# Performance work log

Measured on AMD Instinct MI355X. Metric: run time of the kernel, lower is better.

The kernel has to match this reference:

```python
import jax, jax.numpy as jnp
import numpy as np

C = 512   # in_channels
N = 256   # spatial side (H == W required by the bmm structure)


def setup_inputs() -> dict:
    key = jax.random.key(0)
    kx, kf, kg, kh = jax.random.split(key, 4)
    scale = 1.0 / np.sqrt(C)  # spectral-normalized 1x1 conv weights have ~unit spectral norm
    x = jax.random.normal(kx, (C, N, N), dtype=jnp.float32)
    Wf = jax.random.normal(kf, (C, C), dtype=jnp.float32) * scale  # 1x1 conv kernel squeezed
    Wg = jax.random.normal(kg, (C, C), dtype=jnp.float32) * scale
    Wh = jax.random.normal(kh, (C, C), dtype=jnp.float32) * scale
    return {"x": x, "Wf": Wf, "Wg": Wg, "Wh": Wh}


def reference(x, Wf, Wg, Wh):
    # 1x1 convs (no bias) == channel-mixing matmuls: out[c,h,w] = sum_k W[c,k] x[k,h,w]
    f = jnp.einsum('ck,khw->chw', Wf, x)
    g = jnp.einsum('ck,khw->chw', Wg, x)
    h = jnp.einsum('ck,khw->chw', Wh, x)
    # torch.bmm(f, g): per-channel HxW @ HxW matmul -> [C, N, N]
    scores = jnp.einsum('cik,ckj->cij', f, g)
    # nn.Softmax(dim=1) on [C, N, N] -> softmax over the row axis (axis=1)
    attn_map = jax.nn.softmax(scores, axis=1)
    # torch.bmm(h, attn_map) -> [C, N, N]
    attn = jnp.einsum('cik,ckj->cij', h, attn_map)
    return x + attn
```

## Files before the change

kernel.cpp:

```cpp
#include <hip/hip_runtime.h>

typedef unsigned short u16;
typedef unsigned int   u32;
typedef __attribute__((ext_vector_type(8))) _Float16 half8;
typedef __attribute__((ext_vector_type(4))) float f32x4;
typedef __attribute__((ext_vector_type(2))) float f32x2;
typedef __attribute__((ext_vector_type(4))) u32   u32x4;
typedef __attribute__((ext_vector_type(4))) unsigned short u16x4;

#define MFMAH __builtin_amdgcn_mfma_f32_16x16x32_f16

__device__ u16 W16[786432];

__device__ __forceinline__ u16 f2h(float f) {
  _Float16 h = (_Float16)f;
  union { _Float16 hh; u16 u; } cv; cv.hh = h; return cv.u;
}
__device__ __forceinline__ u32 pkh(float a, float b) {
  return (u32)f2h(a) | ((u32)f2h(b) << 16);
}
__device__ __forceinline__ void gload16(const void* g, void* l) {
  __builtin_amdgcn_global_load_lds(
      (const __attribute__((address_space(1))) void*)g,
      (__attribute__((address_space(3))) void*)l, 16, 0, 0);
}

__global__ __launch_bounds__(256)
void prep_w(const float* __restrict__ Wf, const float* __restrict__ Wg,
            const float* __restrict__ Wh)
{
  const int r = blockIdx.x;
  const int k = threadIdx.x * 2;
  const float* src = (r < 512) ? (Wf + (size_t)r * 512)
                   : (r < 1024) ? (Wg + (size_t)(r - 512) * 512)
                                : (Wh + (size_t)(r - 1024) * 512);
  f32x2 v = *(const f32x2*)(src + k);
  *(u32*)(W16 + (size_t)r * 512 + k) = pkh(v[0], v[1]);
}

__global__ __launch_bounds__(256)
void prep_x(const float* __restrict__ x, u16* __restrict__ x16)
{
  __shared__ float tile[64 * 256];
  const int bk = blockIdx.x & 7, bn = blockIdx.x >> 3;
  const int t = threadIdx.x;
  const int cw = (t & 63) * 4, r0 = (t >> 6) * 16;
#pragma unroll
  for (int it = 0; it < 16; ++it) {
    const int r = r0 + it;
    *(f32x4*)&tile[r * 256 + cw] =
        *(const f32x4*)(x + (size_t)(bk * 64 + r) * 65536 + (size_t)bn * 256 + cw);
  }
  __syncthreads();
  u32 w[32];
#pragma unroll
  for (int q = 0; q < 32; ++q)
    w[q] = pkh(tile[(2 * q) * 256 + t], tile[(2 * q + 1) * 256 + t]);
  const size_t ob = (size_t)(bn * 256 + t) * 512 + bk * 64;
#pragma unroll
  for (int c4 = 0; c4 < 8; ++c4)
    *(u32x4*)(x16 + ob + c4 * 8) = (u32x4){w[4*c4], w[4*c4+1], w[4*c4+2], w[4*c4+3]};
}

__global__ __launch_bounds__(256)
void conv_fgh(const u16* __restrict__ x16, u16* __restrict__ fb,
              u16* __restrict__ gTb, u16* __restrict__ hb)
{
  __shared__ u16 sA[4096], sB[4096];
  const int bid = blockIdx.x;
  const int xcd = bid & 7, idx = bid >> 3;
  const int tn = xcd * 64 + idx / 12;
  const int tm = idx % 12;
  const bool gmode = (tm >= 4) && (tm < 8);
  const int t = threadIdx.x, lane = t & 63, wid = t >> 6;
  const int wr = wid >> 1, wc = wid & 1, lr = lane & 15, lq = lane >> 4;

  const int row0 = t >> 2, row1 = 64 + (t >> 2);
  const int ks0 = (((t & 3) ^ ((row0 >> 1) & 3)) << 3);
  const int ks1 = (((t & 3) ^ ((row1 >> 1) & 3)) << 3);
  const int arA0 = tm * 128 + row0, arA1 = tm * 128 + row1;
  const int bxr0 = gmode ? ((((tn & 1) << 7) + row0) * 256 + (tn >> 1)) : (tn * 128 + row0);
  const int bxr1 = gmode ? ((((tn & 1) << 7) + row1) * 256 + (tn >> 1)) : (tn * 128 + row1);

  int offA[4], offB[4];
#pragma unroll
  for (int mi = 0; mi < 4; ++mi) {
    const int rowA = wr * 64 + mi * 16 + lr;
    offA[mi] = rowA * 32 + ((lq ^ ((rowA >> 1) & 3)) << 3);
  }
#pragma unroll
  for (int ni = 0; ni < 4; ++ni) {
    const int rowB = wc * 64 + ni * 16 + lr;
    offB[ni] = rowB * 32 + ((lq ^ ((rowB >> 1) & 3)) << 3);
  }

  f32x4 acc[4][4] = {};

  for (int k0 = 0; k0 < 512; k0 += 32) {
    gload16(W16 + (size_t)arA0 * 512 + k0 + ks0, (char*)sA + t * 16);
    gload16(W16 + (size_t)arA1 * 512 + k0 + ks1, (char*)sA + 4096 + t * 16);
    gload16(x16 + (size_t)bxr0 * 512 + k0 + ks0, (char*)sB + t * 16);
    gload16(x16 + (size_t)bxr1 * 512 + k0 + ks1, (char*)sB + 4096 + t * 16);
    __syncthreads();
    half8 a[4], b[4];
#pragma unroll
    for (int mi = 0; mi < 4; ++mi) a[mi] = *(const half8*)(sA + offA[mi]);
#pragma unroll
    for (int ni = 0; ni < 4; ++ni) b[ni] = *(const half8*)(sB + offB[ni]);
#pragma unroll
    for (int mi = 0; mi < 4; ++mi)
#pragma unroll
      for (int ni = 0; ni < 4; ++ni)
        acc[mi][ni] = MFMAH(a[mi], b[ni], acc[mi][ni], 0, 0, 0);
    __syncthreads();
  }

  u16* dst = gmode ? gTb : ((tm < 4) ? fb : hb);
  const int mloc = (tm < 4) ? tm : (gmode ? (tm - 4) : (tm - 8));
  const int rbase = mloc * 128 + wr * 64;
  const int cbase = tn * 128 + wc * 64;
#pragma unroll
  for (int mi = 0; mi < 4; ++mi)
#pragma unroll
    for (int ni = 0; ni < 4; ++ni) {
      const int r0 = rbase + mi * 16 + lq * 4;
      const int cc = cbase + ni * 16 + lr;
#pragma unroll
      for (int r = 0; r < 4; ++r)
        dst[(size_t)(r0 + r) * 65536 + cc] = f2h(acc[mi][ni][r]);
    }
}

__global__ __launch_bounds__(512)
void scores_kernel(const u16* __restrict__ fb, const u16* __restrict__ gTb,
                   u16* __restrict__ Pt)
{
  __shared__ u16 sA[8192];
  __shared__ u16 sB[4096];
  __shared__ float cmax[512], csum[512];
  const int bid = blockIdx.x;
  const int xcd = bid & 7, i2 = bid >> 3;
  const int c = xcd * 64 + (i2 >> 1), jt = i2 & 1;
  const size_t cb = (size_t)c * 65536;
  const int t = threadIdx.x, lane = t & 63, wid = t >> 6;
  const int wr = wid >> 1, wc = wid & 1, lr = lane & 15, lq = lane >> 4;

  const int arow0 = t >> 2, arow1 = 128 + (t >> 2);
  const int aks0 = (((t & 3) ^ ((arow0 >> 1) & 3)) << 3);
  const int aks1 = (((t & 3) ^ ((arow1 >> 1) & 3)) << 3);
  const int brow = t >> 2;
  const int bks  = (((t & 3) ^ ((brow >> 1) & 3)) << 3);

  int offA[4], offB[4];
#pragma unroll
  for (int mi = 0; mi < 4; ++mi) {
    const int rowA = wr * 64 + mi * 16 + lr;
    offA[mi] = rowA * 32 + ((lq ^ ((rowA >> 1) & 3)) << 3);
  }
#pragma unroll
  for (int ni = 0; ni < 4; ++ni) {
    const int rowB = wc * 64 + ni * 16 + lr;
    offB[ni] = rowB * 32 + ((lq ^ ((rowB >> 1) & 3)) << 3);
  }

  f32x4 acc[4][4] = {};

  for (int k0 = 0; k0 < 256; k0 += 32) {
    gload16(fb + cb + (size_t)arow0 * 256 + k0 + aks0, (char*)sA + t * 16);
    gload16(fb + cb + (size_t)arow1 * 256 + k0 + aks1, (char*)sA + 8192 + t * 16);
    gload16(gTb + cb + (size_t)(jt * 128 + brow) * 256 + k0 + bks, (char*)sB + t * 16);
    __syncthreads();
    half8 a[4], b[4];
#pragma unroll
    for (int mi = 0; mi < 4; ++mi) a[mi] = *(const half8*)(sA + offA[mi]);
#pragma unroll
    for (int ni = 0; ni < 4; ++ni) b[ni] = *(const half8*)(sB + offB[ni]);
#pragma unroll
    for (int mi = 0; mi < 4; ++mi)
#pragma unroll
      for (int ni = 0; ni < 4; ++ni)
        acc[mi][ni] = MFMAH(a[mi], b[ni], acc[mi][ni], 0, 0, 0);
    __syncthreads();
  }

#pragma unroll
  for (int ni = 0; ni < 4; ++ni) {
    const int col = wc * 64 + ni * 16 + lr;
    float m = -3.4e38f;
#pragma unroll
    for (int mi = 0; mi < 4; ++mi) {
      f32x4 a = acc[mi][ni];
      m = fmaxf(m, fmaxf(fmaxf(a[0], a[1]), fmaxf(a[2], a[3])));
    }
    m = fmaxf(m, __shfl_xor(m, 16));
    m = fmaxf(m, __shfl_xor(m, 32));
    cmax[wr * 128 + col] = m;
  }
  __syncthreads();
#pragma unroll
  for (int ni = 0; ni < 4; ++ni) {
    const int col = wc * 64 + ni * 16 + lr;
    const float M = fmaxf(fmaxf(cmax[col], cmax[128 + col]),
                          fmaxf(cmax[256 + col], cmax[384 + col]));
    float s = 0.f;
#pragma unroll
    for (int mi = 0; mi < 4; ++mi)
#pragma unroll
      for (int r = 0; r < 4; ++r) {
        float e = __expf(acc[mi][ni][r] - M);
        acc[mi][ni][r] = e; s += e;
      }
    s += __shfl_xor(s, 16);
    s += __shfl_xor(s, 32);
    csum[wr * 128 + col] = s;
  }
  __syncthreads();
#pragma unroll
  for (int ni = 0; ni < 4; ++ni) {
    const int col = wc * 64 + ni * 16 + lr;
    const float rs = 1.f / (csum[col] + csum[128 + col] + csum[256 + col] + csum[384 + col]);
    const int j = jt * 128 + col;
#pragma unroll
    for (int mi = 0; mi < 4; ++mi) {
      u16x4 w = { f2h(acc[mi][ni][0] * rs), f2h(acc[mi][ni][1] * rs),
                  f2h(acc[mi][ni][2] * rs), f2h(acc[mi][ni][3] * rs) };
      *(u16x4*)(Pt + cb + (size_t)j * 256 + wr * 64 + mi * 16 + lq * 4) = w;
    }
  }
}

__global__ __launch_bounds__(256)
void attn_kernel(const u16* __restrict__ hb, const u16* __restrict__ Pt,
                 const float* __restrict__ x, float* __restrict__ out)
{
  __shared__ u16 sA[128 * 32], sB[128 * 32];
  const int bid = blockIdx.x;
  const int wg = (bid & 7) * 256 + (bid >> 3);
  const int c = wg >> 2, tm = (wg >> 1) & 1, tn = wg & 1;
  const int t = threadIdx.x, lane = t & 63, wid = t >> 6;
  const int wr = wid >> 1, wc = wid & 1, lr = lane & 15, lq = lane >> 4;
  const size_t cb = (size_t)c * 65536;
  const int grl = t >> 2, gko = t & 3;
  const int ldsb = wid * 1024;

  f32x4 acc[4][4] = {};

  for (int k0 = 0; k0 < 256; k0 += 32) {
#pragma unroll
    for (int q = 0; q < 2; ++q) {
      const int row = q * 64 + grl;
      gload16(hb + cb + (size_t)(tm * 128 + row) * 256 + k0 + gko * 8,
              (char*)sA + q * 4096 + ldsb);
      gload16(Pt + cb + (size_t)(tn * 128 + row) * 256 + k0 + gko * 8,
              (char*)sB + q * 4096 + ldsb);
    }
    __syncthreads();
    half8 af[4], bfr[4];
#pragma unroll
    for (int mi = 0; mi < 4; ++mi)
      af[mi] = *(const half8*)(sA + (wr * 64 + mi * 16 + lr) * 32 + lq * 8);
#pragma unroll
    for (int ni = 0; ni < 4; ++ni)
      bfr[ni] = *(const half8*)(sB + (wc * 64 + ni * 16 + lr) * 32 + lq * 8);
#pragma unroll
    for (int mi = 0; mi < 4; ++mi)
#pragma unroll
      for (int ni = 0; ni < 4; ++ni)
        acc[mi][ni] = MFMAH(af[mi], bfr[ni], acc[mi][ni], 0, 0, 0);
    __syncthreads();
  }

  const float* Xc = x + cb;
  float* Oc = out + cb;
  const int rb = tm * 128 + wr * 64, cbase = tn * 128 + wc * 64;
#pragma unroll
  for (int mi = 0; mi < 4; ++mi)
#pragma unroll
    for (int ni = 0; ni < 4; ++ni) {
      const int r0 = rb + mi * 16 + lq * 4, cc = cbase + ni * 16 + lr;
#pragma unroll
      for (int r = 0; r < 4; ++r) {
        const size_t idx = (size_t)(r0 + r) * 256 + cc;
        Oc[idx] = Xc[idx] + acc[mi][ni][r];
      }
    }
}

extern "C" void kernel_launch(void* const* d_in, const int* in_sizes, int n_in,
                              void* d_out, int out_size, void* d_ws, size_t ws_size,
                              hipStream_t stream)
{
  (void)in_sizes; (void)n_in; (void)out_size; (void)ws_size;
  const float* x  = (const float*)d_in[0];
  const float* Wf = (const float*)d_in[1];
  const float* Wg = (const float*)d_in[2];
  const float* Wh = (const float*)d_in[3];
  float* out = (float*)d_out;
  char*  ws  = (char*)d_ws;

  u16* x16  = (u16*)ws;
  u16* gT16 = (u16*)(ws + 67108864);
  u16* h16  = (u16*)(ws + 134217728);
  u16* f16  = (u16*)d_out;
  u16* Pt   = x16;

  dim3 blk(256, 1, 1);
  prep_w       <<<dim3(1536, 1, 1), blk, 0, stream>>>(Wf, Wg, Wh);
  prep_x       <<<dim3(2048, 1, 1), blk, 0, stream>>>(x, x16);
  conv_fgh     <<<dim3(6144, 1, 1), blk, 0, stream>>>(x16, f16, gT16, h16);
  scores_kernel<<<dim3(1024, 1, 1), dim3(512, 1, 1), 0, stream>>>(f16, gT16, Pt);
  attn_kernel  <<<dim3(2048, 1, 1), blk, 0, stream>>>(h16, Pt, x, out);
}
```

Before: 414.4 us.

## Enlarge conv and attn block tiles to 256x128 with 512 threads sharing B tile

Both the 1x1-conv GEMM and the attention GEMM now launch 512-thread blocks that compute a 256x128 output tile instead of 128x128, so each staged B tile (x16 or Pt) is reused by twice as many output rows. Global-to-LDS traffic per output element drops, and the attn kernel also gains the XOR-swizzled LDS layout already used in the conv kernel to avoid bank conflicts. The cost is half as many blocks, a larger LDS footprint and 512-thread launch bounds, which may lower occupancy or cause register pressure.

```diff
diff --git a/kernel.cpp b/kernel.cpp
--- a/kernel.cpp
+++ b/kernel.cpp
@@ -62,25 +62,26 @@
     *(u32x4*)(x16 + ob + c4 * 8) = (u32x4){w[4*c4], w[4*c4+1], w[4*c4+2], w[4*c4+3]};
 }
 
-__global__ __launch_bounds__(256)
+__global__ __launch_bounds__(512, 4)
 void conv_fgh(const u16* __restrict__ x16, u16* __restrict__ fb,
               u16* __restrict__ gTb, u16* __restrict__ hb)
 {
-  __shared__ u16 sA[4096], sB[4096];
+  __shared__ u16 sA[8192], sB[4096];
   const int bid = blockIdx.x;
   const int xcd = bid & 7, idx = bid >> 3;
-  const int tn = xcd * 64 + idx / 12;
-  const int tm = idx % 12;
-  const bool gmode = (tm >= 4) && (tm < 8);
+  const int tn = xcd * 64 + idx / 6;
+  const int tm2 = idx % 6;
+  const bool gmode = (tm2 >= 2) && (tm2 < 4);
   const int t = threadIdx.x, lane = t & 63, wid = t >> 6;
   const int wr = wid >> 1, wc = wid & 1, lr = lane & 15, lq = lane >> 4;
 
-  const int row0 = t >> 2, row1 = 64 + (t >> 2);
-  const int ks0 = (((t & 3) ^ ((row0 >> 1) & 3)) << 3);
-  const int ks1 = (((t & 3) ^ ((row1 >> 1) & 3)) << 3);
-  const int arA0 = tm * 128 + row0, arA1 = tm * 128 + row1;
-  const int bxr0 = gmode ? ((((tn & 1) << 7) + row0) * 256 + (tn >> 1)) : (tn * 128 + row0);
-  const int bxr1 = gmode ? ((((tn & 1) << 7) + row1) * 256 + (tn >> 1)) : (tn * 128 + row1);
+  const int ar0 = t >> 2, ar1 = 128 + (t >> 2);
+  const int aks0 = (((t & 3) ^ ((ar0 >> 1) & 3)) << 3);
+  const int aks1 = (((t & 3) ^ ((ar1 >> 1) & 3)) << 3);
+  const int garA0 = tm2 * 256 + ar0, garA1 = tm2 * 256 + ar1;
+  const int br = t >> 2;
+  const int bks = (((t & 3) ^ ((br >> 1) & 3)) << 3);
+  const int bxr = gmode ? ((((tn & 1) << 7) + br) * 256 + (tn >> 1)) : (tn * 128 + br);
 
   int offA[4], offB[4];
 #pragma unroll
@@ -97,10 +98,9 @@
   f32x4 acc[4][4] = {};
 
   for (int k0 = 0; k0 < 512; k0 += 32) {
-    gload16(W16 + (size_t)arA0 * 512 + k0 + ks0, (char*)sA + t * 16);
-    gload16(W16 + (size_t)arA1 * 512 + k0 + ks1, (char*)sA + 4096 + t * 16);
-    gload16(x16 + (size_t)bxr0 * 512 + k0 + ks0, (char*)sB + t * 16);
-    gload16(x16 + (size_t)bxr1 * 512 + k0 + ks1, (char*)sB + 4096 + t * 16);
+    gload16(W16 + (size_t)garA0 * 512 + k0 + aks0, (char*)sA + t * 16);
+    gload16(W16 + (size_t)garA1 * 512 + k0 + aks1, (char*)sA + 8192 + t * 16);
+    gload16(x16 + (size_t)bxr * 512 + k0 + bks,    (char*)sB + t * 16);
     __syncthreads();
     half8 a[4], b[4];
 #pragma unroll
@@ -115,9 +115,9 @@
     __syncthreads();
   }
 
-  u16* dst = gmode ? gTb : ((tm < 4) ? fb : hb);
-  const int mloc = (tm < 4) ? tm : (gmode ? (tm - 4) : (tm - 8));
-  const int rbase = mloc * 128 + wr * 64;
+  const int cls = tm2 >> 1;
+  u16* dst = (cls == 0) ? fb : (cls == 1) ? gTb : hb;
+  const int rbase = (tm2 & 1) * 256 + wr * 64;
   const int cbase = tn * 128 + wc * 64;
 #pragma unroll
   for (int mi = 0; mi < 4; ++mi)
@@ -229,55 +229,65 @@
   }
 }
 
-__global__ __launch_bounds__(256)
+__global__ __launch_bounds__(512, 4)
 void attn_kernel(const u16* __restrict__ hb, const u16* __restrict__ Pt,
                  const float* __restrict__ x, float* __restrict__ out)
 {
-  __shared__ u16 sA[128 * 32], sB[128 * 32];
+  __shared__ u16 sA[8192], sB[4096];
   const int bid = blockIdx.x;
-  const int wg = (bid & 7) * 256 + (bid >> 3);
-  const int c = wg >> 2, tm = (wg >> 1) & 1, tn = wg & 1;
+  const int xcd = bid & 7, i2 = bid >> 3;
+  const int c = xcd * 64 + (i2 >> 1), tn = i2 & 1;
+  const size_t cb = (size_t)c * 65536;
   const int t = threadIdx.x, lane = t & 63, wid = t >> 6;
   const int wr = wid >> 1, wc = wid & 1, lr = lane & 15, lq = lane >> 4;
-  const size_t cb = (size_t)c * 65536;
-  const int grl = t >> 2, gko = t & 3;
-  const int ldsb = wid * 1024;
+
+  const int ar0 = t >> 2, ar1 = 128 + (t >> 2);
+  const int aks0 = (((t & 3) ^ ((ar0 >> 1) & 3)) << 3);
+  const int aks1 = (((t & 3) ^ ((ar1 >> 1) & 3)) << 3);
+  const int br = t >> 2;
+  const int bks = (((t & 3) ^ ((br >> 1) & 3)) << 3);
+
+  int offA[4], offB[4];
+#pragma unroll
+  for (int mi = 0; mi < 4; ++mi) {
+    const int rowA = wr * 64 + mi * 16 + lr;
+    offA[mi] = rowA * 32 + ((lq ^ ((rowA >> 1) & 3)) << 3);
+  }
+#pragma unroll
+  for (int ni = 0; ni < 4; ++ni) {
+    const int rowB = wc * 64 + ni * 16 + lr;
+    offB[ni] = rowB * 32 + ((lq ^ ((rowB >> 1) & 3)) << 3);
+  }
 
   f32x4 acc[4][4] = {};
 
   for (int k0 = 0; k0 < 256; k0 += 32) {
-#pragma unroll
-    for (int q = 0; q < 2; ++q) {
-      const int row = q * 64 + grl;
-      gload16(hb + cb + (size_t)(tm * 128 + row) * 256 + k0 + gko * 8,
-              (char*)sA + q * 4096 + ldsb);
-      gload16(Pt + cb + (size_t)(tn * 128 + row) * 256 + k0 + gko * 8,
-              (char*)sB + q * 4096 + ldsb);
-    }
-    __syncthreads();
-    half8 af[4], bfr[4];
+    gload16(hb + cb + (size_t)ar0 * 256 + k0 + aks0, (char*)sA + t * 16);
+    gload16(hb + cb + (size_t)ar1 * 256 + k0 + aks1, (char*)sA + 8192 + t * 16);
+    gload16(Pt + cb + (size_t)(tn * 128 + br) * 256 + k0 + bks, (char*)sB + t * 16);
+    __syncthreads();
+    half8 a[4], b[4];
+#pragma unroll
+    for (int mi = 0; mi < 4; ++mi) a[mi] = *(const half8*)(sA + offA[mi]);
+#pragma unroll
+    for (int ni = 0; ni < 4; ++ni) b[ni] = *(const half8*)(sB + offB[ni]);
 #pragma unroll
     for (int mi = 0; mi < 4; ++mi)
-      af[mi] = *(const half8*)(sA + (wr * 64 + mi * 16 + lr) * 32 + lq * 8);
-#pragma unroll
-    for (int ni = 0; ni < 4; ++ni)
-      bfr[ni] = *(const half8*)(sB + (wc * 64 + ni * 16 + lr) * 32 + lq * 8);
-#pragma unroll
-    for (int mi = 0; mi < 4; ++mi)
 #pragma unroll
       for (int ni = 0; ni < 4; ++ni)
-        acc[mi][ni] = MFMAH(af[mi], bfr[ni], acc[mi][ni], 0, 0, 0);
+        acc[mi][ni] = MFMAH(a[mi], b[ni], acc[mi][ni], 0, 0, 0);
     __syncthreads();
   }
 
   const float* Xc = x + cb;
   float* Oc = out + cb;
-  const int rb = tm * 128 + wr * 64, cbase = tn * 128 + wc * 64;
+  const int rbase = wr * 64;
+  const int cbase = tn * 128 + wc * 64;
 #pragma unroll
   for (int mi = 0; mi < 4; ++mi)
 #pragma unroll
     for (int ni = 0; ni < 4; ++ni) {
-      const int r0 = rb + mi * 16 + lq * 4, cc = cbase + ni * 16 + lr;
+      const int r0 = rbase + mi * 16 + lq * 4, cc = cbase + ni * 16 + lr;
 #pragma unroll
       for (int r = 0; r < 4; ++r) {
         const size_t idx = (size_t)(r0 + r) * 256 + cc;
@@ -307,7 +317,7 @@
   dim3 blk(256, 1, 1);
   prep_w       <<<dim3(1536, 1, 1), blk, 0, stream>>>(Wf, Wg, Wh);
   prep_x       <<<dim3(2048, 1, 1), blk, 0, stream>>>(x, x16);
-  conv_fgh     <<<dim3(6144, 1, 1), blk, 0, stream>>>(x16, f16, gT16, h16);
+  conv_fgh     <<<dim3(3072, 1, 1), dim3(512, 1, 1), 0, stream>>>(x16, f16, gT16, h16);
   scores_kernel<<<dim3(1024, 1, 1), dim3(512, 1, 1), 0, stream>>>(f16, gT16, Pt);
-  attn_kernel  <<<dim3(2048, 1, 1), blk, 0, stream>>>(h16, Pt, x, out);
-}
+  attn_kernel  <<<dim3(1024, 1, 1), dim3(512, 1, 1), 0, stream>>>(h16, Pt, x, out);
+}
```

Result: faster. 354.8 us (-14.4%).
